# Optimization experiments

Measured on AMD Instinct MI355X. Metric: run time of the kernel, lower is better.

## Reference

```python
import jax, jax.numpy as jnp
import numpy as np

B, S = 32, 2048
DIM_ACTION = 32
DIM_STRUCT = 64
HIDDEN = 128  # mlp_hidden_dim default = dim_action * 4
EPS = 1e-12   # F.normalize eps


def l2norm(t):
    n = jnp.linalg.norm(t, axis=-1, keepdims=True)
    return t / jnp.maximum(n, EPS)


def setup_inputs() -> dict:
    key = jax.random.key(0)
    ks = jax.random.split(key, 9)
    sd = lambda fan_in: 1.0 / np.sqrt(fan_in)
    inp = {
        "actions": jax.random.normal(ks[0], (B, S, DIM_ACTION), dtype=jnp.float32),
        # MLP: dim_action -> hidden -> hidden -> dim_structure^2 (depth=2 hidden relu layers)
        "w0": jax.random.uniform(ks[1], (DIM_ACTION, HIDDEN), jnp.float32, -sd(DIM_ACTION), sd(DIM_ACTION)),
        "b0": jnp.zeros((HIDDEN,), jnp.float32),
        "w1": jax.random.uniform(ks[2], (HIDDEN, HIDDEN), jnp.float32, -sd(HIDDEN), sd(HIDDEN)),
        "b1": jnp.zeros((HIDDEN,), jnp.float32),
        "w2": jax.random.uniform(ks[3], (HIDDEN, DIM_STRUCT * DIM_STRUCT), jnp.float32, -sd(HIDDEN), sd(HIDDEN)),
        "b2": jnp.zeros((DIM_STRUCT * DIM_STRUCT,), jnp.float32),
        # RNN init hidden parameter [1, dim_structure], ~N(0, 0.01)
        "init_hidden": jax.random.normal(ks[4], (1, DIM_STRUCT), dtype=jnp.float32) * 0.01,
    }
    return inp


def reference(actions, w0, b0, w1, b1, w2, b2, init_hidden):
    # MLP to transitions: [B, S, d*d]
    h = jax.nn.relu(jnp.einsum("bsa,ah->bsh", actions, w0) + b0)
    h = jax.nn.relu(jnp.einsum("bsh,hk->bsk", h, w1) + b1)
    t = jnp.einsum("bsh,ho->bso", h, w2) + b2
    transitions = t.reshape(B, S, DIM_STRUCT, DIM_STRUCT)  # [B, S, i, j]

    # RNN: hidden_{t+1} = l2norm(relu(hidden_t @ T_t)), scanned over seq
    hidden0 = jnp.broadcast_to(l2norm(init_hidden), (B, DIM_STRUCT))

    def step(hidden, trans):  # trans: [B, i, j]
        hidden = jnp.einsum("bi,bij->bj", hidden, trans)
        hidden = l2norm(jax.nn.relu(hidden))
        return hidden, hidden

    trans_seq = jnp.swapaxes(transitions, 0, 1)  # [S, B, i, j]
    _, hiddens = jax.lax.scan(step, hidden0, trans_seq)  # [S, B, d]
    return jnp.swapaxes(hiddens, 0, 1)  # [B, S, d]
```

## Files before the change

### kernel.cpp

```cpp
#include <hip/hip_runtime.h>

#define B_ 32
#define S_ 2048
#define DA 32
#define DH 128
#define DS 64
#define DS2 4096

typedef _Float16 half8 __attribute__((ext_vector_type(8)));
typedef float f32x4 __attribute__((ext_vector_type(4)));

template <int CTRL>
__device__ __forceinline__ float dpp_add(float x) {
  int t = __builtin_amdgcn_update_dpp(0, __float_as_int(x), CTRL, 0xF, 0xF, true);
  return x + __int_as_float(t);
}
__device__ __forceinline__ float row_sum16(float x) {
  x = dpp_add<0xB1>(x);
  x = dpp_add<0x4E>(x);
  x = dpp_add<0x141>(x);
  x = dpp_add<0x140>(x);
  return x;
}

__device__ __forceinline__ void gl2lds16(const void* g, void* l) {
  __builtin_amdgcn_global_load_lds(
      (const __attribute__((address_space(1))) void*)g,
      (__attribute__((address_space(3))) void*)l, 16, 0, 0);
}

struct SharedGemm {
  _Float16 Ah[128 * 128];
  _Float16 Al[128 * 128];
  _Float16 Bh[128 * 128];
  _Float16 Bl[128 * 128];
};
struct SharedMlp {
  float a_t[DA][64];
  float w0_l[DA][DH];
  float h0t[DH][64];
};
union SharedU {
  SharedGemm g;
  SharedMlp m;
};

__global__ __launch_bounds__(256) void k_split(
    const float* __restrict__ w2, _Float16* __restrict__ w2h,
    _Float16* __restrict__ w2l)
{
  for (int e = blockIdx.x * 256 + threadIdx.x; e < DH * DS2;
       e += gridDim.x * 256) {
    int n = e >> 7, k = e & 127;
    float v = w2[(size_t)k * DS2 + n];
    _Float16 hi = (_Float16)v;
    _Float16 lo = (_Float16)((v - (float)hi) * 2048.0f);
    int kk = k ^ ((n & 7) << 3);
    w2h[(size_t)n * DH + kk] = hi;
    w2l[(size_t)n * DH + kk] = lo;
  }
}

__device__ __forceinline__ void mlp_tile(
    const float* __restrict__ actions, const float* __restrict__ w0,
    const float* __restrict__ b0, const float* __restrict__ w1,
    const float* __restrict__ b1, _Float16* __restrict__ h1h,
    _Float16* __restrict__ h1l, int s_base, int m0, SharedMlp& sm, int tid)
{
#pragma unroll
  for (int q = 0; q < 2; ++q) {
    int g = tid + 256 * q;
    int tok = g >> 3, kq = g & 7;
    int tl = m0 + tok;
    int b = tl & 31, s = s_base + (tl >> 5);
    float4 v = *(const float4*)(actions + ((size_t)b * S_ + s) * DA + 4 * kq);
    sm.a_t[4 * kq + 0][tok] = v.x; sm.a_t[4 * kq + 1][tok] = v.y;
    sm.a_t[4 * kq + 2][tok] = v.z; sm.a_t[4 * kq + 3][tok] = v.w;
  }
#pragma unroll
  for (int q = 0; q < 4; ++q) {
    int g = tid + 256 * q;
    ((float4*)&sm.w0_l[0][0])[g] = ((const float4*)w0)[g];
  }
  __syncthreads();

  const int tm = tid & 15;
  const int tn = tid >> 4;

  float acc[4][8];
#pragma unroll
  for (int mi = 0; mi < 4; ++mi)
#pragma unroll
    for (int ni = 0; ni < 8; ++ni) acc[mi][ni] = 0.f;

#pragma unroll 4
  for (int k = 0; k < DA; ++k) {
    float4 a4 = *(const float4*)&sm.a_t[k][4 * tm];
    float4 wa = *(const float4*)&sm.w0_l[k][8 * tn];
    float4 wb = *(const float4*)&sm.w0_l[k][8 * tn + 4];
    float av[4] = {a4.x, a4.y, a4.z, a4.w};
    float wv[8] = {wa.x, wa.y, wa.z, wa.w, wb.x, wb.y, wb.z, wb.w};
#pragma unroll
    for (int mi = 0; mi < 4; ++mi)
#pragma unroll
      for (int ni = 0; ni < 8; ++ni) acc[mi][ni] += av[mi] * wv[ni];
  }
  {
    float4 ba = *(const float4*)(b0 + 8 * tn);
    float4 bb = *(const float4*)(b0 + 8 * tn + 4);
    float bv[8] = {ba.x, ba.y, ba.z, ba.w, bb.x, bb.y, bb.z, bb.w};
#pragma unroll
    for (int mi = 0; mi < 4; ++mi)
#pragma unroll
      for (int ni = 0; ni < 8; ++ni)
        sm.h0t[8 * tn + ni][4 * tm + mi] = fmaxf(acc[mi][ni] + bv[ni], 0.f);
  }
  __syncthreads();

  float acc1[4][8];
#pragma unroll
  for (int mi = 0; mi < 4; ++mi)
#pragma unroll
    for (int ni = 0; ni < 8; ++ni) acc1[mi][ni] = 0.f;

#pragma unroll 4
  for (int k = 0; k < DH; ++k) {
    float4 h4 = *(const float4*)&sm.h0t[k][4 * tm];
    float4 wa = *(const float4*)(w1 + (size_t)k * DH + 8 * tn);
    float4 wb = *(const float4*)(w1 + (size_t)k * DH + 8 * tn + 4);
    float av[4] = {h4.x, h4.y, h4.z, h4.w};
    float wv[8] = {wa.x, wa.y, wa.z, wa.w, wb.x, wb.y, wb.z, wb.w};
#pragma unroll
    for (int mi = 0; mi < 4; ++mi)
#pragma unroll
      for (int ni = 0; ni < 8; ++ni) acc1[mi][ni] += av[mi] * wv[ni];
  }
  {
    float4 ba = *(const float4*)(b1 + 8 * tn);
    float4 bb = *(const float4*)(b1 + 8 * tn + 4);
    float bv[8] = {ba.x, ba.y, ba.z, ba.w, bb.x, bb.y, bb.z, bb.w};
#pragma unroll
    for (int mi = 0; mi < 4; ++mi) {
      const int m = m0 + 4 * tm + mi;
      half8 hv, lv;
#pragma unroll
      for (int ni = 0; ni < 8; ++ni) {
        float h = fmaxf(acc1[mi][ni] + bv[ni], 0.f);
        _Float16 hi = (_Float16)h;
        hv[ni] = hi;
        lv[ni] = (_Float16)((h - (float)hi) * 2048.0f);
      }
      const int off = m * DH + ((8 * tn) ^ ((m & 7) << 3));
      *(half8*)(h1h + off) = hv;
      *(half8*)(h1l + off) = lv;
    }
  }
}

__device__ __forceinline__ void trans_loop(
    const _Float16* __restrict__ h1h, const _Float16* __restrict__ h1l,
    const _Float16* __restrict__ w2h, const _Float16* __restrict__ w2l,
    const float* __restrict__ b2, float* __restrict__ trans,
    int MT, int x, SharedGemm& sg, int tid)
{
  const int w  = tid >> 6;
  const int lw = tid & 63;
  const int strip = x / 7;
  const int idx   = x % 7;
  const int n0 = strip * 128;

  auto stage32k = [&](const _Float16* src, _Float16* dst) {
    const _Float16* s = src + w * 4096 + lw * 8;
    _Float16* d = dst + w * 4096;
#pragma unroll
    for (int i = 0; i < 8; ++i)
      gl2lds16(s + i * 512, d + i * 512);
  };

  stage32k(w2h + (size_t)n0 * DH, sg.Bh);
  stage32k(w2l + (size_t)n0 * DH, sg.Bl);

  const int fr = lw & 15;
  const int kg = lw >> 4;
  const int wr = w >> 1, wc = w & 1;

  float b2v[4];
#pragma unroll
  for (int fn = 0; fn < 4; ++fn)
    b2v[fn] = b2[n0 + wc * 64 + fn * 16 + fr];

  const f32x4 fz = {0.f, 0.f, 0.f, 0.f};

  for (int mt = idx; mt < MT; mt += 7) {
    const int m0 = mt * 128;
    stage32k(h1h + (size_t)m0 * DH, sg.Ah);
    stage32k(h1l + (size_t)m0 * DH, sg.Al);
    asm volatile("s_waitcnt vmcnt(0)" ::: "memory");
    __syncthreads();

    f32x4 ahh[4][4], axx[4][4], all_[4][4];
#pragma unroll
    for (int fm = 0; fm < 4; ++fm)
#pragma unroll
      for (int fn = 0; fn < 4; ++fn) {
        ahh[fm][fn] = fz;
        axx[fm][fn] = fz;
        all_[fm][fn] = fz;
      }

#pragma unroll
    for (int kc = 0; kc < 4; ++kc) {
      const int k0 = kc * 32 + kg * 8;
      half8 bh[4], bl[4];
#pragma unroll
      for (int fn = 0; fn < 4; ++fn) {
        const int n = wc * 64 + fn * 16 + fr;
        const int off = n * DH + (k0 ^ ((n & 7) << 3));
        bh[fn] = *(const half8*)&sg.Bh[off];
        bl[fn] = *(const half8*)&sg.Bl[off];
      }
#pragma unroll
      for (int fm = 0; fm < 4; ++fm) {
        const int m = wr * 64 + fm * 16 + fr;
        const int off = m * DH + (k0 ^ ((m & 7) << 3));
        half8 ah = *(const half8*)&sg.Ah[off];
        half8 al = *(const half8*)&sg.Al[off];
#pragma unroll
        for (int fn = 0; fn < 4; ++fn) {
          ahh[fm][fn] = __builtin_amdgcn_mfma_f32_16x16x32_f16(
              ah, bh[fn], ahh[fm][fn], 0, 0, 0);
          axx[fm][fn] = __builtin_amdgcn_mfma_f32_16x16x32_f16(
              ah, bl[fn], axx[fm][fn], 0, 0, 0);
          axx[fm][fn] = __builtin_amdgcn_mfma_f32_16x16x32_f16(
              al, bh[fn], axx[fm][fn], 0, 0, 0);
          all_[fm][fn] = __builtin_amdgcn_mfma_f32_16x16x32_f16(
              al, bl[fn], all_[fm][fn], 0, 0, 0);
        }
      }
    }
    __syncthreads();

#pragma unroll
    for (int fm = 0; fm < 4; ++fm) {
#pragma unroll
      for (int fn = 0; fn < 4; ++fn) {
        const int col = n0 + wc * 64 + fn * 16 + fr;
        float* dst = trans +
            (size_t)(m0 + wr * 64 + fm * 16 + kg * 4) * DS2 + col;
#pragma unroll
        for (int r = 0; r < 4; ++r) {
          float v = ahh[fm][fn][r] + axx[fm][fn][r] * (1.0f / 2048.0f) +
                    all_[fm][fn][r] * (1.0f / 4194304.0f) + b2v[fn];
          dst[(size_t)r * DS2] = v;
        }
      }
    }
  }
}

__global__ __launch_bounds__(256) void k_mlp01(
    const float* __restrict__ actions, const float* __restrict__ w0,
    const float* __restrict__ b0, const float* __restrict__ w1,
    const float* __restrict__ b1, _Float16* __restrict__ h1h,
    _Float16* __restrict__ h1l, int s_base)
{
  __shared__ SharedMlp sm;
  mlp_tile(actions, w0, b0, w1, b1, h1h, h1l, s_base, blockIdx.x * 64, sm,
           threadIdx.x);
}

__global__ __launch_bounds__(256, 1) void k_comb(
    const float* __restrict__ actions, const float* __restrict__ w0,
    const float* __restrict__ b0, const float* __restrict__ w1,
    const float* __restrict__ b1, const _Float16* __restrict__ w2h,
    const _Float16* __restrict__ w2l, const float* __restrict__ b2,
    const float* __restrict__ init_hidden,
    float* __restrict__ trans0, float* __restrict__ trans1,
    _Float16* __restrict__ h1h0, _Float16* __restrict__ h1l0,
    _Float16* __restrict__ h1h1, _Float16* __restrict__ h1l1,
    float* __restrict__ hstate, float* __restrict__ out,
    int c, int SC, int nch)
{
  __shared__ SharedU sh;
  const int tid = threadIdx.x;
  const int M = SC * 32;

  if (blockIdx.x >= 32) {
    const int x = blockIdx.x - 32;
    if (c < nch) {
      const _Float16* h1h = (c & 1) ? h1h1 : h1h0;
      const _Float16* h1l = (c & 1) ? h1l1 : h1l0;
      float* trans = (c & 1) ? trans1 : trans0;
      trans_loop(h1h, h1l, w2h, w2l, b2, trans, M / 128, x, sh.g, tid);
      if (c + 1 < nch) {
        __syncthreads();
        _Float16* hh = ((c + 1) & 1) ? h1h1 : h1h0;
        _Float16* hl = ((c + 1) & 1) ? h1l1 : h1l0;
        for (int j = x; j < M / 64; j += 224) {
          mlp_tile(actions, w0, b0, w1, b1, hh, hl, (c + 1) * SC, j * 64,
                   sh.m, tid);
          __syncthreads();
        }
      }
    }
    return;
  }

  if (c == 0) return;
  if (tid >= 64) return;
  const int cc = c - 1;
  const float* trans = (cc & 1) ? trans1 : trans0;
  const int s_base = cc * SC;
  const int lane = tid;
  const int b = blockIdx.x;

  const int d = lane >> 4;
  const int cq = lane & 15;
  const bool d1 = (d & 1), d2 = (d & 2);
  const int pb = lane & 48;

  float4 hq;
  if (cc == 0) {
    hq = *(const float4*)(init_hidden + 4 * cq);
    float ss0 = row_sum16(hq.x * hq.x + hq.y * hq.y + hq.z * hq.z + hq.w * hq.w);
    float iv0 = 1.0f / fmaxf(sqrtf(ss0), 1e-12f);
    hq.x *= iv0; hq.y *= iv0; hq.z *= iv0; hq.w *= iv0;
  } else {
    hq = *(const float4*)(hstate + b * DS + 4 * cq);
  }
  float inv_prev = 1.0f;

  float* outp = out + ((size_t)b * S_ + s_base) * DS + 4 * cq;
  const float* g0 = trans + (size_t)b * DS2 + 4 * lane;
  const size_t sstride = (size_t)32 * DS2;

  auto step_fn = [&](const float4 (&T)[16], int s) {
    float hsel = d2 ? (d1 ? hq.w : hq.z) : (d1 ? hq.y : hq.x);
    float ax = 0.f, ay = 0.f, az = 0.f, aw = 0.f;
#pragma unroll
    for (int q = 0; q < 16; ++q) {
      float hb = __shfl(hsel, pb + q, 64);
      ax += hb * T[q].x; ay += hb * T[q].y;
      az += hb * T[q].z; aw += hb * T[q].w;
    }
    ax += __shfl_xor(ax, 16, 64); ax += __shfl_xor(ax, 32, 64);
    ay += __shfl_xor(ay, 16, 64); ay += __shfl_xor(ay, 32, 64);
    az += __shfl_xor(az, 16, 64); az += __shfl_xor(az, 32, 64);
    aw += __shfl_xor(aw, 16, 64); aw += __shfl_xor(aw, 32, 64);
    hq.x = fmaxf(ax * inv_prev, 0.f);
    hq.y = fmaxf(ay * inv_prev, 0.f);
    hq.z = fmaxf(az * inv_prev, 0.f);
    hq.w = fmaxf(aw * inv_prev, 0.f);
    float ss = row_sum16(hq.x * hq.x + hq.y * hq.y + hq.z * hq.z + hq.w * hq.w);
    float inv = 1.0f / fmaxf(sqrtf(ss), 1e-12f);
    if (d == 0) {
      float4 o;
      o.x = hq.x * inv; o.y = hq.y * inv; o.z = hq.z * inv; o.w = hq.w * inv;
      *(float4*)(outp + (size_t)s * DS) = o;
    }
    inv_prev = inv;
  };

  float4 A[16], Bv[16];
#pragma unroll
  for (int q = 0; q < 16; ++q) A[q] = *(const float4*)(g0 + q * 256);

  for (int s = 0; s < SC; s += 2) {
    const float* g1 = g0 + (size_t)(s + 1) * sstride;
#pragma unroll
    for (int q = 0; q < 16; ++q) Bv[q] = *(const float4*)(g1 + q * 256);
    step_fn(A, s);
    if (s + 2 < SC) {
      const float* g2 = g0 + (size_t)(s + 2) * sstride;
#pragma unroll
      for (int q = 0; q < 16; ++q) A[q] = *(const float4*)(g2 + q * 256);
    }
    step_fn(Bv, s + 1);
  }

  if (d == 0) {
    float4 o;
    o.x = hq.x * inv_prev; o.y = hq.y * inv_prev;
    o.z = hq.z * inv_prev; o.w = hq.w * inv_prev;
    *(float4*)(hstate + b * DS + 4 * cq) = o;
  }
}

extern "C" void kernel_launch(void* const* d_in, const int* in_sizes, int n_in,
                              void* d_out, int out_size, void* d_ws, size_t ws_size,
                              hipStream_t stream) {
  const float* actions     = (const float*)d_in[0];
  const float* w0          = (const float*)d_in[1];
  const float* b0          = (const float*)d_in[2];
  const float* w1          = (const float*)d_in[3];
  const float* b1          = (const float*)d_in[4];
  const float* w2          = (const float*)d_in[5];
  const float* b2          = (const float*)d_in[6];
  const float* init_hidden = (const float*)d_in[7];
  float* out = (float*)d_out;

  int SC = 2048;
  while (SC > 4) {
    size_t need = 2 * (size_t)SC * 32 * DS2 * 4
                + 4 * (size_t)SC * 32 * DH * 2
                + 2 * (size_t)DH * DS2 * 2
                + (size_t)B_ * DS * 4;
    if (need <= ws_size) break;
    SC >>= 1;
  }
  char* p = (char*)d_ws;
  float* trans0 = (float*)p;        p += (size_t)SC * 32 * DS2 * 4;
  float* trans1 = (float*)p;        p += (size_t)SC * 32 * DS2 * 4;
  _Float16* h1h0 = (_Float16*)p;    p += (size_t)SC * 32 * DH * 2;
  _Float16* h1l0 = (_Float16*)p;    p += (size_t)SC * 32 * DH * 2;
  _Float16* h1h1 = (_Float16*)p;    p += (size_t)SC * 32 * DH * 2;
  _Float16* h1l1 = (_Float16*)p;    p += (size_t)SC * 32 * DH * 2;
  _Float16* w2h  = (_Float16*)p;    p += (size_t)DH * DS2 * 2;
  _Float16* w2l  = (_Float16*)p;    p += (size_t)DH * DS2 * 2;
  float* hstate  = (float*)p;

  const int M = SC * 32;
  const int nch = S_ / SC;

  hipLaunchKernelGGL(k_split, dim3(512), dim3(256), 0, stream, w2, w2h, w2l);
  hipLaunchKernelGGL(k_mlp01, dim3(M / 64), dim3(256), 0, stream,
                     actions, w0, b0, w1, b1, h1h0, h1l0, 0);
  for (int c = 0; c <= nch; ++c) {
    hipLaunchKernelGGL(k_comb, dim3(256), dim3(256), 0, stream,
                       actions, w0, b0, w1, b1, w2h, w2l, b2, init_hidden,
                       trans0, trans1, h1h0, h1l0, h1h1, h1l1, hstate, out,
                       c, SC, nch);
  }
}
```

Before: 1.586 ms.

## Stream RNN transition matrices through a 4-slot LDS ring via async global-to-LDS loads

Replaces the register double-buffered transition loads in the RNN scan with a 4-deep LDS ring buffer filled by global_load_lds, keeping three steps of prefetch in flight and using explicit vmcnt waits. The goal is to hide global memory latency on the serial recurrence better than a one-step register prefetch does. In exchange, each step adds LDS reads, and correctness depends on the vmcnt counting and slot reuse. The code has no barrier before a ring slot is refilled, which is only safe if each wave reads only data it loaded itself.

Measured after the change: 2.223 ms. +40.2%, slower.

```diff
diff --git a/kernel.cpp b/kernel.cpp
--- a/kernel.cpp
+++ b/kernel.cpp
@@ -29,6 +29,9 @@
       (__attribute__((address_space(3))) void*)l, 16, 0, 0);
 }
 
+struct SharedRnn {
+  float4 ring[4][16][64];
+};
 struct SharedGemm {
   _Float16 Ah[128 * 128];
   _Float16 Al[128 * 128];
@@ -41,6 +44,7 @@
   float h0t[DH][64];
 };
 union SharedU {
+  SharedRnn r;
   SharedGemm g;
   SharedMlp m;
 };
@@ -331,17 +335,39 @@
   float inv_prev = 1.0f;
 
   float* outp = out + ((size_t)b * S_ + s_base) * DS + 4 * cq;
-  const float* g0 = trans + (size_t)b * DS2 + 4 * lane;
+  const float* gbase = trans + (size_t)b * DS2 + 4 * lane;
   const size_t sstride = (size_t)32 * DS2;
 
-  auto step_fn = [&](const float4 (&T)[16], int s) {
+  auto issue_slot = [&](int s) {
+    const float* g = gbase + (size_t)s * sstride;
+    float* l = (float*)&sh.r.ring[s & 3][0][0];
+#pragma unroll
+    for (int q = 0; q < 16; ++q)
+      gl2lds16(g + q * 256, l + q * 256);
+  };
+
+  issue_slot(0);
+  issue_slot(1);
+  issue_slot(2);
+
+  for (int s = 0; s < SC; ++s) {
+    if (s + 3 < SC) {
+      issue_slot(s + 3);
+      asm volatile("s_waitcnt vmcnt(48)" ::: "memory");
+    } else {
+      asm volatile("s_waitcnt vmcnt(0)" ::: "memory");
+    }
+    __builtin_amdgcn_sched_barrier(0);
+
+    const int slot = s & 3;
     float hsel = d2 ? (d1 ? hq.w : hq.z) : (d1 ? hq.y : hq.x);
     float ax = 0.f, ay = 0.f, az = 0.f, aw = 0.f;
 #pragma unroll
     for (int q = 0; q < 16; ++q) {
+      float4 t4 = sh.r.ring[slot][q][lane];
       float hb = __shfl(hsel, pb + q, 64);
-      ax += hb * T[q].x; ay += hb * T[q].y;
-      az += hb * T[q].z; aw += hb * T[q].w;
+      ax += hb * t4.x; ay += hb * t4.y;
+      az += hb * t4.z; aw += hb * t4.w;
     }
     ax += __shfl_xor(ax, 16, 64); ax += __shfl_xor(ax, 32, 64);
     ay += __shfl_xor(ay, 16, 64); ay += __shfl_xor(ay, 32, 64);
@@ -359,23 +385,6 @@
       *(float4*)(outp + (size_t)s * DS) = o;
     }
     inv_prev = inv;
-  };
-
-  float4 A[16], Bv[16];
-#pragma unroll
-  for (int q = 0; q < 16; ++q) A[q] = *(const float4*)(g0 + q * 256);
-
-  for (int s = 0; s < SC; s += 2) {
-    const float* g1 = g0 + (size_t)(s + 1) * sstride;
-#pragma unroll
-    for (int q = 0; q < 16; ++q) Bv[q] = *(const float4*)(g1 + q * 256);
-    step_fn(A, s);
-    if (s + 2 < SC) {
-      const float* g2 = g0 + (size_t)(s + 2) * sstride;
-#pragma unroll
-      for (int q = 0; q < 16; ++q) A[q] = *(const float4*)(g2 + q * 256);
-    }
-    step_fn(Bv, s + 1);
   }
 
   if (d == 0) {
```
